# Kernel optimization log

Hardware: AMD Instinct MI355X
Metric: run time of the kernel (lower is better)

## Reference

```python
import jax, jax.numpy as jnp
import numpy as np

B, S, D, H, O = 4, 128, 768, 768, 2

def setup_inputs() -> dict:
    key = jax.random.key(0)
    ks = jax.random.split(key, 6)
    scale = 1.0 / np.sqrt(2 * D)
    return {
        "a": jax.random.normal(ks[0], (B, S, D), jnp.float32),
        "b": jax.random.normal(ks[1], (B, S, D), jnp.float32),
        "W1": jax.random.normal(ks[2], (2 * D, H), jnp.float32) * scale,
        "b1": jax.random.normal(ks[3], (H,), jnp.float32) * 0.01,
        "W2": jax.random.normal(ks[4], (H, O), jnp.float32) * (1.0 / np.sqrt(H)),
        "b2": jax.random.normal(ks[5], (O,), jnp.float32) * 0.01,
    }

def reference(a, b, W1, b1, W2, b2):
    # Pairwise concat [a_i ; b_j] followed by Linear(2D->H) is algebraically
    # identical to projecting a and b separately and broadcast-adding
    # (biaffine-style rewrite; same math as cat+matmul, less HBM traffic).
    d = a.shape[-1]
    ha = jnp.einsum('bsd,dh->bsh', a, W1[:d])        # (B, Sa, H)
    hb = jnp.einsum('btd,dh->bth', b, W1[d:])        # (B, Sb, H)
    h = jax.nn.relu(ha[:, :, None, :] + hb[:, None, :, :] + b1)  # (B, Sa, Sb, H)
    scores = jnp.einsum('bsth,ho->bsto', h, W2) + b2  # (B, Sa, Sb, O)
    return scores
```

## Files before the change

kernel.cpp:

```cpp
#include <hip/hip_runtime.h>
#include <hip/hip_fp16.h>


typedef __attribute__((ext_vector_type(2))) _Float16 half2t;
typedef __attribute__((ext_vector_type(8))) _Float16 half8t;
typedef __attribute__((ext_vector_type(4))) float floatx4;
typedef unsigned int uint;

__device__ __forceinline__ half2t pkrtz(float x, float y) {
    __fp16 r __attribute__((ext_vector_type(2))) = __builtin_amdgcn_cvt_pkrtz(x, y);
    half2t o; __builtin_memcpy(&o, &r, 4); return o;
}

__global__ __launch_bounds__(256) void gemm_kernel(
    const float* __restrict__ a, const float* __restrict__ bmat,
    const float* __restrict__ W1, const float* __restrict__ b1,
    ushort* __restrict__ Hf)
{
    const int which = blockIdx.z;
    const int n0 = blockIdx.x * 64;
    const int m0 = blockIdx.y * 64;
    const int t  = threadIdx.x;

    __shared__ ushort As[2][64][72];
    __shared__ ushort Bs[2][64][72];

    const int arow = t >> 2;
    const int akc  = (t & 3) * 16;
    const float* __restrict__ Asrc = which ? bmat : a;
    const float* __restrict__ aptr = Asrc + (size_t)(m0 + arow) * 768 + akc;

    const int ncol = t & 63;
    const int kg   = (t >> 6) * 16;
    const float* __restrict__ bptr = W1 + (size_t)(which * 768 + kg) * 768 + n0 + ncol;

    const int lane = t & 63;
    const int w    = t >> 6;
    const int lr   = lane & 15;
    const int lq   = lane >> 4;

    floatx4 acc0 = {0,0,0,0}, acc1 = {0,0,0,0}, acc2 = {0,0,0,0}, acc3 = {0,0,0,0};

    float4 a4[4];
    float  br[16];
#pragma unroll
    for (int i = 0; i < 4; i++) a4[i] = *(const float4*)(aptr + 4 * i);
#pragma unroll
    for (int j = 0; j < 16; j++) br[j] = bptr[(size_t)j * 768];

    int p = 0;
    for (int kt = 0; kt < 768; kt += 64, p ^= 1) {
        half2t ap[8];
#pragma unroll
        for (int i = 0; i < 4; i++) {
            ap[2 * i    ] = pkrtz(a4[i].x, a4[i].y);
            ap[2 * i + 1] = pkrtz(a4[i].z, a4[i].w);
        }
        __builtin_memcpy(&As[p][arow][akc],     &ap[0], 16);
        __builtin_memcpy(&As[p][arow][akc + 8], &ap[4], 16);
        half2t bp[8];
#pragma unroll
        for (int j = 0; j < 8; j++) bp[j] = pkrtz(br[2 * j], br[2 * j + 1]);
        __builtin_memcpy(&Bs[p][ncol][kg],     &bp[0], 16);
        __builtin_memcpy(&Bs[p][ncol][kg + 8], &bp[4], 16);

        __syncthreads();

        if (kt + 64 < 768) {
#pragma unroll
            for (int i = 0; i < 4; i++)
                a4[i] = *(const float4*)(aptr + kt + 64 + 4 * i);
#pragma unroll
            for (int j = 0; j < 16; j++)
                br[j] = bptr[(size_t)(kt + 64 + j) * 768];
        }

#pragma unroll
        for (int h = 0; h < 2; h++) {
            const int kb = h * 32 + lq * 8;
            half8t bfr, f0, f1, f2, f3;
            __builtin_memcpy(&bfr, &Bs[p][w * 16 + lr][kb], 16);
            __builtin_memcpy(&f0,  &As[p][     lr][kb], 16);
            __builtin_memcpy(&f1,  &As[p][16 + lr][kb], 16);
            __builtin_memcpy(&f2,  &As[p][32 + lr][kb], 16);
            __builtin_memcpy(&f3,  &As[p][48 + lr][kb], 16);
            acc0 = __builtin_amdgcn_mfma_f32_16x16x32_f16(f0, bfr, acc0, 0, 0, 0);
            acc1 = __builtin_amdgcn_mfma_f32_16x16x32_f16(f1, bfr, acc1, 0, 0, 0);
            acc2 = __builtin_amdgcn_mfma_f32_16x16x32_f16(f2, bfr, acc2, 0, 0, 0);
            acc3 = __builtin_amdgcn_mfma_f32_16x16x32_f16(f3, bfr, acc3, 0, 0, 0);
        }
    }

    const int ncolO = n0 + w * 16 + lr;
    const float bias = which ? 0.f : b1[ncolO];
    ushort* __restrict__ dst = Hf + (size_t)which * 393216 + ncolO;
    const int rbase = m0 + lq * 4;
#pragma unroll
    for (int r = 0; r < 4; r++) {
        _Float16 v0 = (_Float16)(acc0[r] + bias);
        _Float16 v1 = (_Float16)(acc1[r] + bias);
        _Float16 v2 = (_Float16)(acc2[r] + bias);
        _Float16 v3 = (_Float16)(acc3[r] + bias);
        ushort u0, u1, u2, u3;
        __builtin_memcpy(&u0, &v0, 2); __builtin_memcpy(&u1, &v1, 2);
        __builtin_memcpy(&u2, &v2, 2); __builtin_memcpy(&u3, &v3, 2);
        dst[(size_t)(rbase +      r) * 768] = u0;
        dst[(size_t)(rbase + 16 + r) * 768] = u1;
        dst[(size_t)(rbase + 32 + r) * 768] = u2;
        dst[(size_t)(rbase + 48 + r) * 768] = u3;
    }
}

__global__ __launch_bounds__(256) void pair_kernel(
    const ushort* __restrict__ Hf, const float* __restrict__ W2,
    const float* __restrict__ b2, float* __restrict__ out)
{
    const int bb = blockIdx.z;
    const int s0 = blockIdx.y * 16;
    const int t0 = blockIdx.x * 16;
    const int tid = threadIdx.x;

    __shared__ ushort hAs[16][776];
    __shared__ ushort hBs[16][776];
    __shared__ uint w2s[768];

    const ushort* __restrict__ Asrc = Hf +          (size_t)(bb * 128 + s0) * 768;
    const ushort* __restrict__ Bsrc = Hf + 393216 + (size_t)(bb * 128 + t0) * 768;

#pragma unroll
    for (int i = 0; i < 6; i++) {
        const int c   = tid + i * 256;
        const int row = c / 96;
        const int col = (c % 96) * 8;
        *(uint4*)&hAs[row][col] = *(const uint4*)(Asrc + (size_t)row * 768 + col);
        *(uint4*)&hBs[row][col] = *(const uint4*)(Bsrc + (size_t)row * 768 + col);
    }
#pragma unroll
    for (int j = tid; j < 768; j += 256) {
        const int o  = (j >= 384) ? 1 : 0;
        const int h2 = j - o * 384;
        half2t p = pkrtz(W2[4 * h2 + o], W2[4 * h2 + 2 + o]);
        uint u; __builtin_memcpy(&u, &p, 4);
        w2s[j] = u;
    }
    __syncthreads();

    const int sl = tid >> 4;
    const int tl = tid & 15;
    const ushort* __restrict__ arow = &hAs[sl][0];
    const ushort* __restrict__ brow = &hBs[tl][0];

    float acc0 = 0.f, acc1 = 0.f;
    const half2t zero = {(_Float16)0.f, (_Float16)0.f};

#pragma unroll 8
    for (int h8 = 0; h8 < 768; h8 += 8) {
        half2t pa[4], pb[4], w0[4], w1[4];
        __builtin_memcpy(pa, arow + h8, 16);
        __builtin_memcpy(pb, brow + h8, 16);
        __builtin_memcpy(w0, &w2s[h8 / 2], 16);
        __builtin_memcpy(w1, &w2s[384 + h8 / 2], 16);
#pragma unroll
        for (int j = 0; j < 4; j++) {
            half2t s = pa[j] + pb[j];
            s = __builtin_elementwise_max(s, zero);
            acc0 = __builtin_amdgcn_fdot2(s, w0[j], acc0, false);
            acc1 = __builtin_amdgcn_fdot2(s, w1[j], acc1, false);
        }
    }

    const int sg = bb * 128 + s0 + sl;
    const int tg = t0 + tl;
    float2 r = make_float2(acc0 + b2[0], acc1 + b2[1]);
    *(float2*)&out[((size_t)sg * 128 + tg) * 2] = r;
}

extern "C" void kernel_launch(void* const* d_in, const int* in_sizes, int n_in,
                              void* d_out, int out_size, void* d_ws, size_t ws_size,
                              hipStream_t stream) {
    const float* a  = (const float*)d_in[0];
    const float* b  = (const float*)d_in[1];
    const float* W1 = (const float*)d_in[2];
    const float* b1 = (const float*)d_in[3];
    const float* W2 = (const float*)d_in[4];
    const float* b2 = (const float*)d_in[5];
    float* out = (float*)d_out;

    ushort* Hf = (ushort*)d_ws;

    gemm_kernel<<<dim3(12, 8, 2), 256, 0, stream>>>(a, b, W1, b1, Hf);
    pair_kernel<<<dim3(8, 8, 4), 256, 0, stream>>>(Hf, W2, b2, out);
}
```

Measured before the change: 88.99 us.

## Fuse projection GEMM and pair kernel into one launch with a flag-based grid barrier

Merges the two kernels into a single 256-block kernel. The first 192 blocks compute the fp16 projections into the workspace, then every block publishes a done flag and spins until all 256 flags are set before running the pairwise ReLU/dot phase. This removes the second launch and the gap between the two kernels. It relies on all 256 blocks being resident at the same time. The flags are never reset, so on later calls the barrier may pass immediately and the pair phase could read stale projections left from an earlier call.

```diff
diff --git a/kernel.cpp b/kernel.cpp
--- a/kernel.cpp
+++ b/kernel.cpp
@@ -7,172 +7,197 @@
 typedef __attribute__((ext_vector_type(4))) float floatx4;
 typedef unsigned int uint;
 
+#define DONE_FLAG 0x600DF00Du
+
 __device__ __forceinline__ half2t pkrtz(float x, float y) {
     __fp16 r __attribute__((ext_vector_type(2))) = __builtin_amdgcn_cvt_pkrtz(x, y);
     half2t o; __builtin_memcpy(&o, &r, 4); return o;
 }
 
-__global__ __launch_bounds__(256) void gemm_kernel(
+__global__ __launch_bounds__(256) void fused_kernel(
     const float* __restrict__ a, const float* __restrict__ bmat,
     const float* __restrict__ W1, const float* __restrict__ b1,
-    ushort* __restrict__ Hf)
+    const float* __restrict__ W2, const float* __restrict__ b2,
+    ushort* __restrict__ Hf,
+    uint* __restrict__ flags,
+    float* __restrict__ out)
 {
-    const int which = blockIdx.z;
-    const int n0 = blockIdx.x * 64;
-    const int m0 = blockIdx.y * 64;
-    const int t  = threadIdx.x;
-
-    __shared__ ushort As[2][64][72];
-    __shared__ ushort Bs[2][64][72];
-
-    const int arow = t >> 2;
-    const int akc  = (t & 3) * 16;
-    const float* __restrict__ Asrc = which ? bmat : a;
-    const float* __restrict__ aptr = Asrc + (size_t)(m0 + arow) * 768 + akc;
-
-    const int ncol = t & 63;
-    const int kg   = (t >> 6) * 16;
-    const float* __restrict__ bptr = W1 + (size_t)(which * 768 + kg) * 768 + n0 + ncol;
-
-    const int lane = t & 63;
-    const int w    = t >> 6;
-    const int lr   = lane & 15;
-    const int lq   = lane >> 4;
-
-    floatx4 acc0 = {0,0,0,0}, acc1 = {0,0,0,0}, acc2 = {0,0,0,0}, acc3 = {0,0,0,0};
-
-    float4 a4[4];
-    float  br[16];
-#pragma unroll
-    for (int i = 0; i < 4; i++) a4[i] = *(const float4*)(aptr + 4 * i);
-#pragma unroll
-    for (int j = 0; j < 16; j++) br[j] = bptr[(size_t)j * 768];
-
-    int p = 0;
-    for (int kt = 0; kt < 768; kt += 64, p ^= 1) {
-        half2t ap[8];
-#pragma unroll
-        for (int i = 0; i < 4; i++) {
-            ap[2 * i    ] = pkrtz(a4[i].x, a4[i].y);
-            ap[2 * i + 1] = pkrtz(a4[i].z, a4[i].w);
-        }
-        __builtin_memcpy(&As[p][arow][akc],     &ap[0], 16);
-        __builtin_memcpy(&As[p][arow][akc + 8], &ap[4], 16);
-        half2t bp[8];
-#pragma unroll
-        for (int j = 0; j < 8; j++) bp[j] = pkrtz(br[2 * j], br[2 * j + 1]);
-        __builtin_memcpy(&Bs[p][ncol][kg],     &bp[0], 16);
-        __builtin_memcpy(&Bs[p][ncol][kg + 8], &bp[4], 16);
-
+    __shared__ __align__(16) char smem[52736];
+    const int blk = blockIdx.x;
+    const int t   = threadIdx.x;
+
+    if (blk < 192) {
+        const int which = blk / 96;
+        const int rem   = blk % 96;
+        const int n0 = (rem % 12) * 64;
+        const int m0 = (rem / 12) * 64;
+
+        ushort* As = (ushort*)smem;
+        ushort* Bs = As + 2 * 64 * 72;
+        #define AS(pp,r,c) As[(((pp) * 64) + (r)) * 72 + (c)]
+        #define BS(pp,r,c) Bs[(((pp) * 64) + (r)) * 72 + (c)]
+
+        const int arow = t >> 2;
+        const int akc  = (t & 3) * 16;
+        const float* __restrict__ Asrc = which ? bmat : a;
+        const float* __restrict__ aptr = Asrc + (size_t)(m0 + arow) * 768 + akc;
+
+        const int ncol = t & 63;
+        const int kg   = (t >> 6) * 16;
+        const float* __restrict__ bptr = W1 + (size_t)(which * 768 + kg) * 768 + n0 + ncol;
+
+        const int lane = t & 63;
+        const int w    = t >> 6;
+        const int lr   = lane & 15;
+        const int lq   = lane >> 4;
+
+        floatx4 acc0 = {0,0,0,0}, acc1 = {0,0,0,0}, acc2 = {0,0,0,0}, acc3 = {0,0,0,0};
+
+        float4 a4[4];
+        float  br[16];
+#pragma unroll
+        for (int i = 0; i < 4; i++) a4[i] = *(const float4*)(aptr + 4 * i);
+#pragma unroll
+        for (int j = 0; j < 16; j++) br[j] = bptr[(size_t)j * 768];
+
+        int p = 0;
+        for (int kt = 0; kt < 768; kt += 64, p ^= 1) {
+            half2t ap[8];
+#pragma unroll
+            for (int i = 0; i < 4; i++) {
+                ap[2 * i    ] = pkrtz(a4[i].x, a4[i].y);
+                ap[2 * i + 1] = pkrtz(a4[i].z, a4[i].w);
+            }
+            __builtin_memcpy(&AS(p, arow, akc),     &ap[0], 16);
+            __builtin_memcpy(&AS(p, arow, akc + 8), &ap[4], 16);
+            half2t bp[8];
+#pragma unroll
+            for (int j = 0; j < 8; j++) bp[j] = pkrtz(br[2 * j], br[2 * j + 1]);
+            __builtin_memcpy(&BS(p, ncol, kg),     &bp[0], 16);
+            __builtin_memcpy(&BS(p, ncol, kg + 8), &bp[4], 16);
+
+            __syncthreads();
+
+            if (kt + 64 < 768) {
+#pragma unroll
+                for (int i = 0; i < 4; i++)
+                    a4[i] = *(const float4*)(aptr + kt + 64 + 4 * i);
+#pragma unroll
+                for (int j = 0; j < 16; j++)
+                    br[j] = bptr[(size_t)(kt + 64 + j) * 768];
+            }
+
+#pragma unroll
+            for (int h = 0; h < 2; h++) {
+                const int kb = h * 32 + lq * 8;
+                half8t bfr, f0, f1, f2, f3;
+                __builtin_memcpy(&bfr, &BS(p, w * 16 + lr, kb), 16);
+                __builtin_memcpy(&f0,  &AS(p,      lr, kb), 16);
+                __builtin_memcpy(&f1,  &AS(p, 16 + lr, kb), 16);
+                __builtin_memcpy(&f2,  &AS(p, 32 + lr, kb), 16);
+                __builtin_memcpy(&f3,  &AS(p, 48 + lr, kb), 16);
+                acc0 = __builtin_amdgcn_mfma_f32_16x16x32_f16(f0, bfr, acc0, 0, 0, 0);
+                acc1 = __builtin_amdgcn_mfma_f32_16x16x32_f16(f1, bfr, acc1, 0, 0, 0);
+                acc2 = __builtin_amdgcn_mfma_f32_16x16x32_f16(f2, bfr, acc2, 0, 0, 0);
+                acc3 = __builtin_amdgcn_mfma_f32_16x16x32_f16(f3, bfr, acc3, 0, 0, 0);
+            }
+        }
+        #undef AS
+        #undef BS
+
+        const int ncolO = n0 + w * 16 + lr;
+        const float bias = which ? 0.f : b1[ncolO];
+        ushort* __restrict__ dst = Hf + (size_t)which * 393216 + ncolO;
+        const int rbase = m0 + lq * 4;
+#pragma unroll
+        for (int r = 0; r < 4; r++) {
+            _Float16 v0 = (_Float16)(acc0[r] + bias);
+            _Float16 v1 = (_Float16)(acc1[r] + bias);
+            _Float16 v2 = (_Float16)(acc2[r] + bias);
+            _Float16 v3 = (_Float16)(acc3[r] + bias);
+            ushort u0, u1, u2, u3;
+            __builtin_memcpy(&u0, &v0, 2); __builtin_memcpy(&u1, &v1, 2);
+            __builtin_memcpy(&u2, &v2, 2); __builtin_memcpy(&u3, &v3, 2);
+            dst[(size_t)(rbase +      r) * 768] = u0;
+            dst[(size_t)(rbase + 16 + r) * 768] = u1;
+            dst[(size_t)(rbase + 32 + r) * 768] = u2;
+            dst[(size_t)(rbase + 48 + r) * 768] = u3;
+        }
+    }
+
+    __threadfence();
+    __syncthreads();
+    if (t == 0)
+        __hip_atomic_store(&flags[blk], DONE_FLAG, __ATOMIC_RELEASE,
+                           __HIP_MEMORY_SCOPE_AGENT);
+    for (;;) {
+        uint v = __hip_atomic_load(&flags[t], __ATOMIC_ACQUIRE,
+                                   __HIP_MEMORY_SCOPE_AGENT);
+        if (__syncthreads_and(v == DONE_FLAG)) break;
+        __builtin_amdgcn_s_sleep(8);
+    }
+    __threadfence();
+
+    {
+        const int bb  = blk >> 6;
+        const int rem = blk & 63;
+        const int s0 = (rem >> 3) * 16;
+        const int t0 = (rem & 7) * 16;
+
+        ushort* hAs = (ushort*)smem;
+        ushort* hBs = hAs + 16 * 776;
+        uint*   w2s = (uint*)(hBs + 16 * 776);
+
+        const ushort* __restrict__ Asrc2 = Hf +          (size_t)(bb * 128 + s0) * 768;
+        const ushort* __restrict__ Bsrc2 = Hf + 393216 + (size_t)(bb * 128 + t0) * 768;
+
+#pragma unroll
+        for (int i = 0; i < 6; i++) {
+            const int c   = t + i * 256;
+            const int row = c / 96;
+            const int col = (c % 96) * 8;
+            *(uint4*)&hAs[row * 776 + col] = *(const uint4*)(Asrc2 + (size_t)row * 768 + col);
+            *(uint4*)&hBs[row * 776 + col] = *(const uint4*)(Bsrc2 + (size_t)row * 768 + col);
+        }
+#pragma unroll
+        for (int j = t; j < 768; j += 256) {
+            const int o  = (j >= 384) ? 1 : 0;
+            const int h2 = j - o * 384;
+            half2t pw = pkrtz(W2[4 * h2 + o], W2[4 * h2 + 2 + o]);
+            uint u; __builtin_memcpy(&u, &pw, 4);
+            w2s[j] = u;
+        }
         __syncthreads();
 
-        if (kt + 64 < 768) {
-#pragma unroll
-            for (int i = 0; i < 4; i++)
-                a4[i] = *(const float4*)(aptr + kt + 64 + 4 * i);
-#pragma unroll
-            for (int j = 0; j < 16; j++)
-                br[j] = bptr[(size_t)(kt + 64 + j) * 768];
-        }
-
-#pragma unroll
-        for (int h = 0; h < 2; h++) {
-            const int kb = h * 32 + lq * 8;
-            half8t bfr, f0, f1, f2, f3;
-            __builtin_memcpy(&bfr, &Bs[p][w * 16 + lr][kb], 16);
-            __builtin_memcpy(&f0,  &As[p][     lr][kb], 16);
-            __builtin_memcpy(&f1,  &As[p][16 + lr][kb], 16);
-            __builtin_memcpy(&f2,  &As[p][32 + lr][kb], 16);
-            __builtin_memcpy(&f3,  &As[p][48 + lr][kb], 16);
-            acc0 = __builtin_amdgcn_mfma_f32_16x16x32_f16(f0, bfr, acc0, 0, 0, 0);
-            acc1 = __builtin_amdgcn_mfma_f32_16x16x32_f16(f1, bfr, acc1, 0, 0, 0);
-            acc2 = __builtin_amdgcn_mfma_f32_16x16x32_f16(f2, bfr, acc2, 0, 0, 0);
-            acc3 = __builtin_amdgcn_mfma_f32_16x16x32_f16(f3, bfr, acc3, 0, 0, 0);
-        }
+        const int sl = t >> 4;
+        const int tl = t & 15;
+        const ushort* __restrict__ arow2 = &hAs[sl * 776];
+        const ushort* __restrict__ brow2 = &hBs[tl * 776];
+
+        float acc0 = 0.f, acc1 = 0.f;
+        const half2t zero = {(_Float16)0.f, (_Float16)0.f};
+
+#pragma unroll 8
+        for (int h8 = 0; h8 < 768; h8 += 8) {
+            half2t pa[4], pb[4], w0[4], w1[4];
+            __builtin_memcpy(pa, arow2 + h8, 16);
+            __builtin_memcpy(pb, brow2 + h8, 16);
+            __builtin_memcpy(w0, &w2s[h8 / 2], 16);
+            __builtin_memcpy(w1, &w2s[384 + h8 / 2], 16);
+#pragma unroll
+            for (int j = 0; j < 4; j++) {
+                half2t s = pa[j] + pb[j];
+                s = __builtin_elementwise_max(s, zero);
+                acc0 = __builtin_amdgcn_fdot2(s, w0[j], acc0, false);
+                acc1 = __builtin_amdgcn_fdot2(s, w1[j], acc1, false);
+            }
+        }
+
+        const int sg = bb * 128 + s0 + sl;
+        const int tg = t0 + tl;
+        float2 r = make_float2(acc0 + b2[0], acc1 + b2[1]);
+        *(float2*)&out[((size_t)sg * 128 + tg) * 2] = r;
     }
-
-    const int ncolO = n0 + w * 16 + lr;
-    const float bias = which ? 0.f : b1[ncolO];
-    ushort* __restrict__ dst = Hf + (size_t)which * 393216 + ncolO;
-    const int rbase = m0 + lq * 4;
-#pragma unroll
-    for (int r = 0; r < 4; r++) {
-        _Float16 v0 = (_Float16)(acc0[r] + bias);
-        _Float16 v1 = (_Float16)(acc1[r] + bias);
-        _Float16 v2 = (_Float16)(acc2[r] + bias);
-        _Float16 v3 = (_Float16)(acc3[r] + bias);
-        ushort u0, u1, u2, u3;
-        __builtin_memcpy(&u0, &v0, 2); __builtin_memcpy(&u1, &v1, 2);
-        __builtin_memcpy(&u2, &v2, 2); __builtin_memcpy(&u3, &v3, 2);
-        dst[(size_t)(rbase +      r) * 768] = u0;
-        dst[(size_t)(rbase + 16 + r) * 768] = u1;
-        dst[(size_t)(rbase + 32 + r) * 768] = u2;
-        dst[(size_t)(rbase + 48 + r) * 768] = u3;
-    }
-}
-
-__global__ __launch_bounds__(256) void pair_kernel(
-    const ushort* __restrict__ Hf, const float* __restrict__ W2,
-    const float* __restrict__ b2, float* __restrict__ out)
-{
-    const int bb = blockIdx.z;
-    const int s0 = blockIdx.y * 16;
-    const int t0 = blockIdx.x * 16;
-    const int tid = threadIdx.x;
-
-    __shared__ ushort hAs[16][776];
-    __shared__ ushort hBs[16][776];
-    __shared__ uint w2s[768];
-
-    const ushort* __restrict__ Asrc = Hf +          (size_t)(bb * 128 + s0) * 768;
-    const ushort* __restrict__ Bsrc = Hf + 393216 + (size_t)(bb * 128 + t0) * 768;
-
-#pragma unroll
-    for (int i = 0; i < 6; i++) {
-        const int c   = tid + i * 256;
-        const int row = c / 96;
-        const int col = (c % 96) * 8;
-        *(uint4*)&hAs[row][col] = *(const uint4*)(Asrc + (size_t)row * 768 + col);
-        *(uint4*)&hBs[row][col] = *(const uint4*)(Bsrc + (size_t)row * 768 + col);
-    }
-#pragma unroll
-    for (int j = tid; j < 768; j += 256) {
-        const int o  = (j >= 384) ? 1 : 0;
-        const int h2 = j - o * 384;
-        half2t p = pkrtz(W2[4 * h2 + o], W2[4 * h2 + 2 + o]);
-        uint u; __builtin_memcpy(&u, &p, 4);
-        w2s[j] = u;
-    }
-    __syncthreads();
-
-    const int sl = tid >> 4;
-    const int tl = tid & 15;
-    const ushort* __restrict__ arow = &hAs[sl][0];
-    const ushort* __restrict__ brow = &hBs[tl][0];
-
-    float acc0 = 0.f, acc1 = 0.f;
-    const half2t zero = {(_Float16)0.f, (_Float16)0.f};
-
-#pragma unroll 8
-    for (int h8 = 0; h8 < 768; h8 += 8) {
-        half2t pa[4], pb[4], w0[4], w1[4];
-        __builtin_memcpy(pa, arow + h8, 16);
-        __builtin_memcpy(pb, brow + h8, 16);
-        __builtin_memcpy(w0, &w2s[h8 / 2], 16);
-        __builtin_memcpy(w1, &w2s[384 + h8 / 2], 16);
-#pragma unroll
-        for (int j = 0; j < 4; j++) {
-            half2t s = pa[j] + pb[j];
-            s = __builtin_elementwise_max(s, zero);
-            acc0 = __builtin_amdgcn_fdot2(s, w0[j], acc0, false);
-            acc1 = __builtin_amdgcn_fdot2(s, w1[j], acc1, false);
-        }
-    }
-
-    const int sg = bb * 128 + s0 + sl;
-    const int tg = t0 + tl;
-    float2 r = make_float2(acc0 + b2[0], acc1 + b2[1]);
-    *(float2*)&out[((size_t)sg * 128 + tg) * 2] = r;
 }
 
 extern "C" void kernel_launch(void* const* d_in, const int* in_sizes, int n_in,
@@ -186,8 +211,8 @@
     const float* b2 = (const float*)d_in[5];
     float* out = (float*)d_out;
 
-    ushort* Hf = (ushort*)d_ws;
-
-    gemm_kernel<<<dim3(12, 8, 2), 256, 0, stream>>>(a, b, W1, b1, Hf);
-    pair_kernel<<<dim3(8, 8, 4), 256, 0, stream>>>(Hf, W2, b2, out);
+    ushort* Hf   = (ushort*)d_ws;
+    uint*  flags = (uint*)((char*)d_ws + (4 << 20));
+
+    fused_kernel<<<256, 256, 0, stream>>>(a, b, W1, b1, W2, b2, Hf, flags, out);
 }
```

Result: slower. 164.4 us (+84.7%).

## Read pair operands directly from global memory and prepack W2 in GEMM kernel

Applied to the files above, without the earlier changes.

The pair kernel no longer stages the two 16-row H tiles and packed W2 in shared memory behind a barrier. Each thread now streams its own rows of the projected activations and the prepacked W2 straight from global memory. W2 is packed into fp16 pairs once by a single block of the GEMM kernel and written to workspace. This removes the shared-memory fill, the barrier and the LDS footprint, but relies on L1/L2 caching for row reuse across the 16 threads that share a row. The global loads per thread are strided by 768 halves, so they coalesce poorly.

```diff
diff --git a/kernel.cpp b/kernel.cpp
--- a/kernel.cpp
+++ b/kernel.cpp
@@ -15,12 +15,25 @@
 __global__ __launch_bounds__(256) void gemm_kernel(
     const float* __restrict__ a, const float* __restrict__ bmat,
     const float* __restrict__ W1, const float* __restrict__ b1,
-    ushort* __restrict__ Hf)
+    const float* __restrict__ W2,
+    ushort* __restrict__ Hf,
+    uint* __restrict__ W2pk)
 {
     const int which = blockIdx.z;
     const int n0 = blockIdx.x * 64;
     const int m0 = blockIdx.y * 64;
     const int t  = threadIdx.x;
+
+    if (blockIdx.x == 0 && blockIdx.y == 0 && which == 0) {
+#pragma unroll
+        for (int j = t; j < 768; j += 256) {
+            const int o  = (j >= 384) ? 1 : 0;
+            const int h2 = j - o * 384;
+            half2t p = pkrtz(W2[4 * h2 + o], W2[4 * h2 + 2 + o]);
+            uint u; __builtin_memcpy(&u, &p, 4);
+            W2pk[j] = u;
+        }
+    }
 
     __shared__ ushort As[2][64][72];
     __shared__ ushort Bs[2][64][72];
@@ -112,43 +125,18 @@
 }
 
 __global__ __launch_bounds__(256) void pair_kernel(
-    const ushort* __restrict__ Hf, const float* __restrict__ W2,
+    const ushort* __restrict__ Hf, const uint* __restrict__ W2pk,
     const float* __restrict__ b2, float* __restrict__ out)
 {
     const int bb = blockIdx.z;
     const int s0 = blockIdx.y * 16;
     const int t0 = blockIdx.x * 16;
     const int tid = threadIdx.x;
-
-    __shared__ ushort hAs[16][776];
-    __shared__ ushort hBs[16][776];
-    __shared__ uint w2s[768];
-
-    const ushort* __restrict__ Asrc = Hf +          (size_t)(bb * 128 + s0) * 768;
-    const ushort* __restrict__ Bsrc = Hf + 393216 + (size_t)(bb * 128 + t0) * 768;
-
-#pragma unroll
-    for (int i = 0; i < 6; i++) {
-        const int c   = tid + i * 256;
-        const int row = c / 96;
-        const int col = (c % 96) * 8;
-        *(uint4*)&hAs[row][col] = *(const uint4*)(Asrc + (size_t)row * 768 + col);
-        *(uint4*)&hBs[row][col] = *(const uint4*)(Bsrc + (size_t)row * 768 + col);
-    }
-#pragma unroll
-    for (int j = tid; j < 768; j += 256) {
-        const int o  = (j >= 384) ? 1 : 0;
-        const int h2 = j - o * 384;
-        half2t p = pkrtz(W2[4 * h2 + o], W2[4 * h2 + 2 + o]);
-        uint u; __builtin_memcpy(&u, &p, 4);
-        w2s[j] = u;
-    }
-    __syncthreads();
-
     const int sl = tid >> 4;
     const int tl = tid & 15;
-    const ushort* __restrict__ arow = &hAs[sl][0];
-    const ushort* __restrict__ brow = &hBs[tl][0];
+
+    const ushort* __restrict__ arow = Hf +          (size_t)(bb * 128 + s0 + sl) * 768;
+    const ushort* __restrict__ brow = Hf + 393216 + (size_t)(bb * 128 + t0 + tl) * 768;
 
     float acc0 = 0.f, acc1 = 0.f;
     const half2t zero = {(_Float16)0.f, (_Float16)0.f};
@@ -158,8 +146,8 @@
         half2t pa[4], pb[4], w0[4], w1[4];
         __builtin_memcpy(pa, arow + h8, 16);
         __builtin_memcpy(pb, brow + h8, 16);
-        __builtin_memcpy(w0, &w2s[h8 / 2], 16);
-        __builtin_memcpy(w1, &w2s[384 + h8 / 2], 16);
+        __builtin_memcpy(w0, &W2pk[h8 / 2],       16);
+        __builtin_memcpy(w1, &W2pk[384 + h8 / 2], 16);
 #pragma unroll
         for (int j = 0; j < 4; j++) {
             half2t s = pa[j] + pb[j];
@@ -186,8 +174,9 @@
     const float* b2 = (const float*)d_in[5];
     float* out = (float*)d_out;
 
-    ushort* Hf = (ushort*)d_ws;
+    ushort* Hf   = (ushort*)d_ws;
+    uint*   W2pk = (uint*)((char*)d_ws + (2 << 20));
 
-    gemm_kernel<<<dim3(12, 8, 2), 256, 0, stream>>>(a, b, W1, b1, Hf);
-    pair_kernel<<<dim3(8, 8, 4), 256, 0, stream>>>(Hf, W2, b2, out);
+    gemm_kernel<<<dim3(12, 8, 2), 256, 0, stream>>>(a, b, W1, b1, W2, Hf, W2pk);
+    pair_kernel<<<dim3(8, 8, 4), 256, 0, stream>>>(Hf, W2pk, b2, out);
 }
```

Measured after the change: 96.92 us. 8.9% more time.
